# Kernel optimization log

Measured on AMD Instinct MI355X. Metric: run time of the kernel, lower is better.

## Reference

```python
import jax, jax.numpy as jnp
import numpy as np

DIM = 128; DSTATE = 64; DHEAD = 64; EXPAND = 2
DINNER = EXPAND * DIM; NH = DINNER // DHEAD
CONVK = 4; CHUNK = 128
BATCH = 1; DD = 32; HH = 32; WW = 32
CONVCH = DINNER + 2 * DSTATE
DPROJ = 2 * DINNER + 2 * DSTATE + NH


def rmsnorm(v, w, eps=1e-6):
    return v * jax.lax.rsqrt(jnp.mean(v * v, axis=-1, keepdims=True) + eps) * w


def ssd(xh, dt, A, Bm, Cm):
    # chunked SSD selective scan. xh [b,l,h,p], dt [b,l,h], A [h], Bm/Cm [b,l,n]
    b, l, h, p = xh.shape
    n = Bm.shape[-1]
    c, k = l // CHUNK, CHUNK
    dA = (dt * A).reshape(b, c, k, h)
    xdt = (xh * dt[..., None]).reshape(b, c, k, h, p)
    Bm = Bm.reshape(b, c, k, n)
    Cm = Cm.reshape(b, c, k, n)
    cum = jnp.cumsum(dA, axis=2)                  # [b,c,k,h] inclusive
    cum_h = cum.transpose(0, 1, 3, 2)             # [b,c,h,k]
    tri = jnp.tril(jnp.ones((k, k), bool))
    Lmat = jnp.exp(jnp.where(tri, cum_h[..., :, None] - cum_h[..., None, :], -jnp.inf))
    CB = jnp.einsum('bctn,bcsn->bcts', Cm, Bm)
    Y_intra = jnp.einsum('bcts,bchts,bcshp->bcthp', CB, Lmat, xdt)
    decay_end = jnp.exp(cum[:, :, -1:, :] - cum)  # [b,c,k,h]
    S = jnp.einsum('bcsn,bcsh,bcshp->bchpn', Bm, decay_end, xdt)
    cdec = jnp.exp(cum[:, :, -1])                 # [b,c,h]

    def step(hprev, inp):
        s_c, dec = inp
        return dec[:, :, None, None] * hprev + s_c, hprev

    init = jnp.zeros((b, h, p, n), xh.dtype)
    _, hprevs = jax.lax.scan(step, init, (S.transpose(1, 0, 2, 3, 4), cdec.transpose(1, 0, 2)))
    hprevs = hprevs.transpose(1, 0, 2, 3, 4)      # [b,c,h,p,n] state at each chunk start
    Y_inter = jnp.einsum('bctn,bcth,bchpn->bcthp', Cm, jnp.exp(cum), hprevs)
    return (Y_intra + Y_inter).reshape(b, l, h, p)


def mamba2(x, Win, convw, convb, dtb, Alog, Dp, normw, Wout):
    b, l, _ = x.shape
    zxbcdt = x @ Win
    z = zxbcdt[..., :DINNER]
    xBC = zxbcdt[..., DINNER:DINNER + CONVCH]
    dt = zxbcdt[..., DINNER + CONVCH:]
    xc = xBC.transpose(0, 2, 1)
    xc = jax.lax.conv_general_dilated(xc, convw, (1,), [(CONVK - 1, 0)],
                                      dimension_numbers=('NCH', 'OIH', 'NCH'),
                                      feature_group_count=CONVCH)
    xBC = jax.nn.silu(xc + convb[None, :, None]).transpose(0, 2, 1)
    xh = xBC[..., :DINNER].reshape(b, l, NH, DHEAD)
    Bm = xBC[..., DINNER:DINNER + DSTATE]
    Cm = xBC[..., DINNER + DSTATE:]
    dt = jax.nn.softplus(dt + dtb)
    A = -jnp.exp(Alog)
    y = ssd(xh, dt, A, Bm, Cm) + Dp[None, None, :, None] * xh
    y = y.reshape(b, l, DINNER)
    y = rmsnorm(y * jax.nn.silu(z), normw)
    return y @ Wout


def ss3d(xn, gate_w, gate_b, ps, pn, pz):
    B, D, H, W, C = xn.shape
    x_s = xn.reshape(B, -1, C)
    x_n = jnp.transpose(xn, (0, 2, 1, 3, 4)).reshape(B, -1, C)
    x_z = jnp.transpose(xn, (0, 3, 1, 2, 4)).reshape(B, -1, C)
    o_sf = mamba2(x_s, *ps).reshape(B, D, H, W, C)
    o_sb = jnp.flip(mamba2(jnp.flip(x_s, 1), *ps), 1).reshape(B, D, H, W, C)
    o_nf = mamba2(x_n, *pn).reshape(B, H, D, W, C).transpose(0, 2, 1, 3, 4)
    o_nb = jnp.flip(mamba2(jnp.flip(x_n, 1), *pn), 1).reshape(B, H, D, W, C).transpose(0, 2, 1, 3, 4)
    o_zf = mamba2(x_z, *pz).reshape(B, W, D, H, C).transpose(0, 2, 3, 1, 4)
    o_zb = jnp.flip(mamba2(jnp.flip(x_z, 1), *pz), 1).reshape(B, W, D, H, C).transpose(0, 2, 3, 1, 4)
    stack = jnp.stack([o_sf, o_sb, o_nf, o_nb, o_zf, o_zb], axis=1)  # [B,6,D,H,W,C]
    gates = jax.nn.softmax(xn @ gate_w + gate_b, axis=-1)            # [B,D,H,W,6]
    gates = jnp.transpose(gates[..., None], (0, 4, 1, 2, 3, 5))      # [B,6,D,H,W,1]
    return (stack * gates).sum(axis=1)


def block(x, norm_w, gate_w, gate_b, ps, pn, pz, loc_dw_w, loc_dw_b, loc_pw_w, loc_pw_b,
          ca_w1, ca_b1, ca_w2, ca_b2, alpha):
    xp = jnp.transpose(x, (0, 2, 3, 4, 1))
    xn = rmsnorm(xp, norm_w)
    g = jnp.transpose(ss3d(xn, gate_w, gate_b, ps, pn, pz), (0, 4, 1, 2, 3))
    xcf = jnp.transpose(xn, (0, 4, 1, 2, 3))
    lc = jax.lax.conv_general_dilated(xcf, loc_dw_w, (1, 1, 1), [(1, 1)] * 3,
                                      dimension_numbers=('NCDHW', 'OIDHW', 'NCDHW'),
                                      feature_group_count=DIM) + loc_dw_b[None, :, None, None, None]
    lc = jax.nn.silu(jnp.einsum('bcdhw,oc->bodhw', lc, loc_pw_w) + loc_pw_b[None, :, None, None, None])
    fused = alpha * g + (1.0 - alpha) * lc
    yc = jnp.mean(fused, axis=(2, 3, 4), keepdims=True)
    yc = jnp.einsum('bcdhw,oc->bodhw', yc, ca_w1) + ca_b1[None, :, None, None, None]
    yc = jnp.where(yc >= 0, yc, 0.1 * yc)  # LeakyReLU(0.1)
    yc = jnp.einsum('bcdhw,oc->bodhw', yc, ca_w2) + ca_b2[None, :, None, None, None]
    return x + fused * jax.nn.sigmoid(yc)


def setup_inputs() -> dict:
    keys = iter(jax.random.split(jax.random.key(0), 64))

    def rn(shape, s=1.0):
        return jax.random.normal(next(keys), shape, jnp.float32) * s

    inp = {"x": rn((BATCH, DIM, DD, HH, WW))}
    inp["norm_w"] = jnp.ones((DIM,)) + rn((DIM,), 0.02)
    inp["gate_w"] = rn((DIM, 6), 0.02)
    inp["gate_b"] = jnp.zeros((6,))
    for m in ("s", "n", "zm"):
        inp[m + "_Win"] = rn((DIM, DPROJ), 0.02)
        inp[m + "_convw"] = rn((CONVCH, 1, CONVK), 0.2)
        inp[m + "_convb"] = jnp.zeros((CONVCH,))
        inp[m + "_dtb"] = rn((NH,), 0.3)
        inp[m + "_Alog"] = jnp.log(jnp.arange(1, NH + 1, dtype=jnp.float32))
        inp[m + "_D"] = jnp.ones((NH,))
        inp[m + "_normw"] = jnp.ones((DINNER,))
        inp[m + "_Wout"] = rn((DINNER, DIM), 0.02)
    inp["loc_dw_w"] = rn((DIM, 1, 3, 3, 3), 0.1)
    inp["loc_dw_b"] = jnp.zeros((DIM,))
    inp["loc_pw_w"] = rn((DIM, DIM), 0.05)
    inp["loc_pw_b"] = jnp.zeros((DIM,))
    inp["ca_w1"] = rn((DIM // 16, DIM), 0.05)
    inp["ca_b1"] = jnp.zeros((DIM // 16,))
    inp["ca_w2"] = rn((DIM, DIM // 16), 0.05)
    inp["ca_b2"] = jnp.zeros((DIM,))
    inp["alpha"] = jnp.array(0.5, jnp.float32)
    return inp


def reference(x, norm_w, gate_w, gate_b,
              s_Win, s_convw, s_convb, s_dtb, s_Alog, s_D, s_normw, s_Wout,
              n_Win, n_convw, n_convb, n_dtb, n_Alog, n_D, n_normw, n_Wout,
              zm_Win, zm_convw, zm_convb, zm_dtb, zm_Alog, zm_D, zm_normw, zm_Wout,
              loc_dw_w, loc_dw_b, loc_pw_w, loc_pw_b, ca_w1, ca_b1, ca_w2, ca_b2, alpha):
    ps = (s_Win, s_convw, s_convb, s_dtb, s_Alog, s_D, s_normw, s_Wout)
    pn = (n_Win, n_convw, n_convb, n_dtb, n_Alog, n_D, n_normw, n_Wout)
    pz = (zm_Win, zm_convw, zm_convb, zm_dtb, zm_Alog, zm_D, zm_normw, zm_Wout)
    return block(x, norm_w, gate_w, gate_b, ps, pn, pz,
                 loc_dw_w, loc_dw_b, loc_pw_w, loc_pw_b, ca_w1, ca_b1, ca_w2, ca_b2, alpha)
```

## Files before the change

### kernel.cpp

```cpp
#include <hip/hip_runtime.h>


typedef unsigned short u16;
typedef unsigned int   u32;
typedef __attribute__((ext_vector_type(8))) short short8;
typedef __attribute__((ext_vector_type(8))) _Float16 half8;
typedef __attribute__((ext_vector_type(4))) float f32x4;

#define LSEQ 32768
#define CDIM 128
#define NPROJ 644
#define CCH 384
#define DIN 256
#define NHD 4
#define CKL 128
#define NCHK 256

__device__ __forceinline__ float b2f(u16 u){ u32 x=((u32)u)<<16; float f; __builtin_memcpy(&f,&x,4); return f; }
__device__ __forceinline__ u16 f2b(float f){ u32 x; __builtin_memcpy(&x,&f,4); x += 0x7fffu + ((x>>16)&1u); return (u16)(x>>16); }
__device__ __forceinline__ u16 f2h(float v){ _Float16 h=(_Float16)v; u16 b; __builtin_memcpy(&b,&h,2); return b; }
__device__ __forceinline__ float h2f(u16 b){ _Float16 h; __builtin_memcpy(&h,&b,2); return (float)h; }
__device__ __forceinline__ void up4(uint2 v, float* o){
  union { uint2 u; _Float16 h[4]; } c; c.u = v;
  o[0]=(float)c.h[0]; o[1]=(float)c.h[1]; o[2]=(float)c.h[2]; o[3]=(float)c.h[3];
}
__device__ __forceinline__ uint2 pk4(const float* o){
  union { uint2 u; _Float16 h[4]; } c;
  c.h[0]=(_Float16)o[0]; c.h[1]=(_Float16)o[1]; c.h[2]=(_Float16)o[2]; c.h[3]=(_Float16)o[3];
  return c.u;
}
__device__ __forceinline__ float sigmoidf_(float v){ return 1.f/(1.f+__expf(-v)); }
__device__ __forceinline__ float siluf_(float v){ return v*sigmoidf_(v); }
__device__ __forceinline__ float softplusf_(float v){ return (v>20.f)? v : log1pf(__expf(v)); }

__device__ __forceinline__ int seq2sp(int t, int run){
  int te = (run&1) ? (LSEQ-1-t) : t;
  int a = te>>10, b=(te>>5)&31, c=te&31;
  int d,h,w;
  switch(run>>1){
    case 0: d=a; h=b; w=c; break;
    case 1: h=a; d=b; w=c; break;
    default: w=a; d=b; h=c; break;
  }
  return (d<<10)|(h<<5)|w;
}

__global__ void k_xn(const float* __restrict__ x, const float* __restrict__ nw,
                     const float* __restrict__ gw, const float* __restrict__ gb,
                     float* __restrict__ XN, float* __restrict__ G){
  int s = blockIdx.x*256 + threadIdx.x;
  float ss = 0.f;
  #pragma unroll 8
  for (int c=0;c<CDIM;c++){ float v=x[c*LSEQ+s]; ss += v*v; }
  float sc = rsqrtf(ss*(1.f/CDIM)+1e-6f);
  float a[6];
  #pragma unroll
  for (int j=0;j<6;j++) a[j]=gb[j];
  #pragma unroll 8
  for (int c=0;c<CDIM;c++){
    float v = x[c*LSEQ+s]*sc*nw[c];
    XN[c*LSEQ+s] = v;
    #pragma unroll
    for (int j=0;j<6;j++) a[j] += v*gw[c*6+j];
  }
  float m=a[0];
  #pragma unroll
  for (int j=1;j<6;j++) m = fmaxf(m,a[j]);
  float e[6], ssum=0.f;
  #pragma unroll
  for (int j=0;j<6;j++){ e[j]=__expf(a[j]-m); ssum+=e[j]; }
  float inv = 1.f/ssum;
  #pragma unroll
  for (int j=0;j<6;j++) G[j*LSEQ+s] = e[j]*inv;
}

__global__ __launch_bounds__(256) void k_permute(const float* __restrict__ XN, u16* __restrict__ XNT, int dir){
  __shared__ u16 TS[128*34];
  int a = blockIdx.x>>5, b = blockIdx.x&31;
  int tid = threadIdx.x;
  int spa = (dir==1)? b : a;
  int spb = (dir==1)? a : b;
  int spbase = spa*1024 + spb*32;
  for (int idx=tid; idx<4096; idx+=256){
    int c = idx>>5, i = idx&31;
    TS[c*34+i] = f2b(XN[c*LSEQ + spbase + i]);
  }
  __syncthreads();
  for (int idx=tid; idx<4096; idx+=256){
    int i = idx>>7, c = idx&127;
    int t = (dir==2) ? (i*1024 + a*32 + b) : (a*1024 + b*32 + i);
    XNT[t*128 + c] = TS[c*34+i];
  }
}

__global__ void k_prep(const float* __restrict__ Win, const float* __restrict__ Wout,
                       u16* __restrict__ WinT, u16* __restrict__ WoT){
  int bid = blockIdx.x;
  if (bid < 384){
    int idx = bid*256 + threadIdx.x;
    int j = idx>>7, k = idx&127;
    float v = (j<NPROJ)? Win[k*NPROJ + j] : 0.f;
    WinT[idx] = f2b(v);
  } else {
    int idx = (bid-384)*256 + threadIdx.x;
    int c = idx>>8, k = idx&255;
    WoT[idx] = f2h(Wout[k*CDIM + c]);
  }
}

__global__ __launch_bounds__(256) void k_gin_mfma(const u16* __restrict__ XNT, const u16* __restrict__ WinT,
                                                  u16* __restrict__ ZX, int flip){
  __shared__ u16 Asb[128*136];
  __shared__ u16 Bsb[128*136];
  int j0 = blockIdx.x*128, t0 = blockIdx.y*128;
  int tid = threadIdx.x;
  for (int ch = tid; ch < 2048; ch += 256){
    int row = ch>>4, c8 = ch&15;
    int tg = flip ? (LSEQ-1-(t0+row)) : (t0+row);
    uint4 av = *(const uint4*)(XNT + tg*128 + c8*8);
    *(uint4*)(&Asb[row*136 + c8*8]) = av;
    uint4 bv = *(const uint4*)(WinT + (j0+row)*128 + c8*8);
    *(uint4*)(&Bsb[row*136 + c8*8]) = bv;
  }
  __syncthreads();
  int lane = tid&63, wid = tid>>6;
  int wm = (wid>>1)*64, wn = (wid&1)*64;
  int lm = lane&15, lq = lane>>4;
  f32x4 acc[4][4] = {};
  for (int kt=0; kt<4; kt++){
    short8 af[4], bf[4];
    #pragma unroll
    for (int mt=0;mt<4;mt++) af[mt] = *(const short8*)(&Asb[(wm+mt*16+lm)*136 + kt*32 + lq*8]);
    #pragma unroll
    for (int nt=0;nt<4;nt++) bf[nt] = *(const short8*)(&Bsb[(wn+nt*16+lm)*136 + kt*32 + lq*8]);
    #pragma unroll
    for (int mt=0;mt<4;mt++)
      #pragma unroll
      for (int nt=0;nt<4;nt++)
        acc[mt][nt] = __builtin_amdgcn_mfma_f32_16x16x32_bf16(af[mt], bf[nt], acc[mt][nt], 0,0,0);
  }
  #pragma unroll
  for (int mt=0;mt<4;mt++){
    #pragma unroll
    for (int nt=0;nt<4;nt++){
      int j = j0 + wn + nt*16 + lm;
      if (j < NPROJ){
        #pragma unroll
        for (int r=0;r<4;r++){
          int t = t0 + wm + mt*16 + lq*4 + r;
          ZX[t*NPROJ + j] = f2h(acc[mt][nt][r]);
        }
      }
    }
  }
}

__global__ __launch_bounds__(384) void k_conv(const u16* __restrict__ ZX, const float* __restrict__ cw,
                                              const float* __restrict__ cb, u16* __restrict__ XB){
  __shared__ u16 smc[35*384];
  int t0 = blockIdx.x*32;
  int tid = threadIdx.x;
  for (int idx=tid; idx<13440; idx+=384){
    int j = idx/384, chh = idx - j*384;
    int t = t0-3+j;
    smc[idx] = (t>=0)? ZX[t*NPROJ + 256 + chh] : (u16)0;
  }
  __syncthreads();
  int ch = tid;
  float w0=cw[ch*4], w1=cw[ch*4+1], w2=cw[ch*4+2], w3=cw[ch*4+3], bb=cb[ch];
  for (int i=0;i<32;i++){
    float acc = w0*h2f(smc[i*384+ch]) + w1*h2f(smc[(i+1)*384+ch])
              + w2*h2f(smc[(i+2)*384+ch]) + w3*h2f(smc[(i+3)*384+ch]) + bb;
    XB[(t0+i)*CCH + ch] = f2h(siluf_(acc));
  }
}

__global__ __launch_bounds__(256) void k_dtcum(const u16* __restrict__ ZX, const float* __restrict__ dtb,
                                               const float* __restrict__ Alog, float* __restrict__ DT,
                                               float* __restrict__ CUM, float* __restrict__ CDEC,
                                               float* __restrict__ DE){
  int g = blockIdx.x*4 + (threadIdx.x>>6);
  int lane = threadIdx.x&63;
  int c = g>>2, h = g&3;
  float A = -__expf(Alog[h]);
  float bias = dtb[h];
  int t0 = c*CKL + lane*2;
  float x0 = h2f(ZX[t0*NPROJ + 640 + h]);
  float x1 = h2f(ZX[(t0+1)*NPROJ + 640 + h]);
  float d0 = softplusf_(x0+bias), d1 = softplusf_(x1+bias);
  DT[t0*4+h] = d0; DT[(t0+1)*4+h] = d1;
  float e0 = d0*A, e1 = d1*A;
  float s = e0+e1;
  #pragma unroll
  for (int off=1; off<64; off<<=1){
    float v = __shfl_up(s, off, 64);
    if (lane>=off) s += v;
  }
  float c0 = s - e1, c1 = s;
  CUM[t0*4+h] = c0;
  CUM[(t0+1)*4+h] = c1;
  float tot = __shfl(s, 63, 64);
  DE[t0*4+h]     = __expf(tot - c0);
  DE[(t0+1)*4+h] = __expf(tot - c1);
  if (lane==0) CDEC[c*4+h] = __expf(tot);
}

__global__ __launch_bounds__(256,4) void k_chunk(const u16* __restrict__ XB, const float* __restrict__ DT,
                                                 const float* __restrict__ CUM, const float* __restrict__ DE,
                                                 const float* __restrict__ Dp,
                                                 u16* __restrict__ YA, u16* __restrict__ ST){
  __shared__ u16 sh[19968];
  u16* R0   = sh;
  u16* Mtri = sh;
  u16* Xsh  = sh + 11264;

  int bid = blockIdx.x; int c = bid&255, h = bid>>8;
  int tid = threadIdx.x, lane = tid&63, wid = tid>>6;
  int lm = lane&15, lq = lane>>4;
  const u16* XBc = XB + c*CKL*CCH;
  const float* DTc = DT + c*CKL*4 + h;
  const float* DEc = DE + c*CKL*4 + h;

  for (int idx=tid; idx<4096; idx+=256){
    int t2 = idx>>6, n = idx&63, t = t2*2;
    const u16* r0 = XBc + t*CCH;
    float dt0 = DTc[t*4], dt1 = DTc[(t+1)*4];
    u32 xp = (u32)f2h(h2f(r0[(h<<6)+n])*dt0) | ((u32)f2h(h2f(r0[CCH+(h<<6)+n])*dt1)<<16);
    *(u32*)&Xsh[n*136 + t] = xp;
    float de0 = DEc[t*4], de1 = DEc[(t+1)*4];
    u32 bp = (u32)f2h(h2f(r0[256+n])*de0) | ((u32)f2h(h2f(r0[CCH+256+n])*de1)<<16);
    *(u32*)&R0[n*136 + t] = bp;
  }
  if (tid<128) ((float*)(Xsh + (tid>>1)*136 + 128))[tid&1] = CUM[(c*CKL+tid)*4 + h];
  __syncthreads();
  #define CUMS(t) (((const float*)(Xsh + ((t)>>1)*136 + 128))[(t)&1])

  f32x4 sa[4] = {};
  #pragma unroll
  for (int kt=0; kt<4; kt++){
    half8 aa = *(const half8*)&Xsh[(wid*16+lm)*136 + kt*32 + lq*8];
    #pragma unroll
    for (int nt=0;nt<4;nt++){
      half8 bq = *(const half8*)&R0[(nt*16+lm)*136 + kt*32 + lq*8];
      sa[nt] = __builtin_amdgcn_mfma_f32_16x16x32_f16(aa, bq, sa[nt], 0,0,0);
    }
  }
  #pragma unroll
  for (int nt=0;nt<4;nt++){
    int n = nt*16 + lm;
    #pragma unroll
    for (int r=0;r<4;r++){
      int p = wid*16 + lq*4 + r;
      ST[((c*4+h)*64 + p)*64 + n] = f2h(sa[nt][r]);
    }
  }

  int sp0 = wid, sp1 = 7 - wid;
  f32x4 cbA[4] = {};
  f32x4 cbB[8] = {};
  const u16* lanebase = XBc + lm*CCH + lq*8;
  #pragma unroll
  for (int kt=0; kt<2; kt++){
    half8 afA = *(const half8*)(lanebase + sp0*16*CCH + 320 + kt*32);
    half8 afB = *(const half8*)(lanebase + sp1*16*CCH + 320 + kt*32);
    #pragma unroll
    for (int st=0; st<8; st++){
      if (st <= sp1){
        half8 bq = *(const half8*)(lanebase + st*16*CCH + 256 + kt*32);
        if (st <= sp0)
          cbA[st&3] = __builtin_amdgcn_mfma_f32_16x16x32_f16(afA, bq, cbA[st&3], 0,0,0);
        cbB[st] = __builtin_amdgcn_mfma_f32_16x16x32_f16(afB, bq, cbB[st], 0,0,0);
      }
    }
  }
  __syncthreads();

  float dval = Dp[h];
  #pragma unroll
  for (int i=0;i<2;i++){
    int sp_ = i ? sp1 : sp0;
    int q = sp_ >> 1;
    int Wst = 32*q + 40;
    int mb  = 16*(32*q*q + 48*q + (sp_&1)*(32*q+40));
    u16* Mrow = Mtri + mb;
    float ct[4];
    #pragma unroll
    for (int r=0;r<4;r++) ct[r] = CUMS(sp_*16 + lq*4 + r);

    #pragma unroll
    for (int st=0; st<8; st++){
      if (st <= sp_){
        int s = st*16 + lm;
        float cs = CUMS(s);
        f32x4 cb;
        if (i==0) cb = cbA[st&3]; else cb = cbB[st];
        if (st == sp_){
          #pragma unroll
          for (int r=0;r<4;r++){
            int t = sp_*16 + lq*4 + r;
            float m = (s <= t) ? cb[r]*__expf(ct[r]-cs) : 0.f;
            Mrow[(lq*4+r)*Wst + s] = f2h(m);
          }
          if (!(sp_&1)){
            #pragma unroll
            for (int r=0;r<4;r++) Mrow[(lq*4+r)*Wst + s + 16] = 0;
          }
        } else {
          #pragma unroll
          for (int r=0;r<4;r++)
            Mrow[(lq*4+r)*Wst + s] = f2h(cb[r]*__expf(ct[r]-cs));
        }
      }
    }

    f32x4 ya[4] = {};
    int nkt = q + 1;
    #pragma unroll
    for (int kt=0; kt<4; kt++){
      if (kt < nkt){
        half8 af = *(const half8*)&Mrow[lm*Wst + kt*32 + lq*8];
        #pragma unroll
        for (int nt=0;nt<4;nt++){
          half8 bq = *(const half8*)&Xsh[(nt*16+lm)*136 + kt*32 + lq*8];
          ya[nt] = __builtin_amdgcn_mfma_f32_16x16x32_f16(af, bq, ya[nt], 0,0,0);
        }
      }
    }

    #pragma unroll
    for (int nt=0;nt<4;nt++){
      int p = nt*16 + lm;
      #pragma unroll
      for (int r=0;r<4;r++){
        int t = sp_*16 + lq*4 + r;
        float xhv = h2f(XBc[t*CCH + (h<<6) + p]);
        YA[((c*CKL+t)<<8) + (h<<6) + p] = f2h(ya[nt][r] + dval*xhv);
      }
    }
  }
  #undef CUMS
}

__global__ void k_scan(const u16* __restrict__ ST, u16* __restrict__ HP, const float* __restrict__ CDEC){
  int g = blockIdx.x*256 + threadIdx.x;
  int h = g>>12;
  float hp = 0.f;
  #pragma unroll 32
  for (int c=0;c<NCHK;c++){
    float dec = CDEC[(c<<2)+h];
    float sv = h2f(ST[g + (c<<14)]);
    HP[g + (c<<14)] = f2h(hp);
    hp = dec*hp + sv;
  }
}

__global__ __launch_bounds__(256) void k_inter(const u16* __restrict__ XB, const float* __restrict__ CUM,
                                               const u16* __restrict__ HP, u16* __restrict__ YB){
  __shared__ u16 Cs[128*72];
  __shared__ u16 Hs[4*64*72];
  __shared__ float ex_s[4*128];
  int c = blockIdx.x;
  int tid = threadIdx.x, lane = tid&63, wid = tid>>6;
  int lm = lane&15, lq = lane>>4;
  for (int idx=tid; idx<1024; idx+=256){
    int t = idx>>3, b8 = idx&7;
    *(uint4*)&Cs[t*72 + b8*8] = *(const uint4*)(XB + (c*CKL+t)*CCH + 320 + b8*8);
  }
  for (int idx=tid; idx<2048; idx+=256){
    int h = idx>>9, p = (idx>>3)&63, b8 = idx&7;
    *(uint4*)&Hs[(h*64+p)*72 + b8*8] = *(const uint4*)(HP + ((c*4+h)*64+p)*64 + b8*8);
  }
  for (int idx=tid; idx<512; idx+=256){
    int h = idx>>7, t = idx&127;
    ex_s[h*128+t] = __expf(CUM[(c*CKL+t)*4+h]);
  }
  __syncthreads();
  int h = wid;
  const u16* Hh = &Hs[h*64*72];
  f32x4 acc[8][4] = {};
  for (int kt=0; kt<2; kt++){
    half8 af[8], bfv[4];
    #pragma unroll
    for (int mt=0;mt<8;mt++) af[mt] = *(const half8*)&Cs[(mt*16+lm)*72 + kt*32 + lq*8];
    #pragma unroll
    for (int nt=0;nt<4;nt++) bfv[nt] = *(const half8*)&Hh[(nt*16+lm)*72 + kt*32 + lq*8];
    #pragma unroll
    for (int mt=0;mt<8;mt++)
      #pragma unroll
      for (int nt=0;nt<4;nt++)
        acc[mt][nt] = __builtin_amdgcn_mfma_f32_16x16x32_f16(af[mt], bfv[nt], acc[mt][nt], 0,0,0);
  }
  #pragma unroll
  for (int mt=0;mt<8;mt++){
    #pragma unroll
    for (int r=0;r<4;r++){
      int t = mt*16 + lq*4 + r;
      float e = ex_s[h*128+t];
      u16* dst = &YB[((c*CKL+t)<<8) + (h<<6)];
      #pragma unroll
      for (int nt=0;nt<4;nt++){
        int p = nt*16 + lm;
        dst[p] = f2h(e*acc[mt][nt][r]);
      }
    }
  }
}

__global__ __launch_bounds__(256) void k_gout_mfma(const u16* __restrict__ YA, const u16* __restrict__ YB,
                                                   const u16* __restrict__ ZX, const float* __restrict__ nw,
                                                   const u16* __restrict__ WoT,
                                                   const float* __restrict__ G, float* __restrict__ GACC, int run){
  __shared__ u16 Ys[128*136];
  __shared__ u16 Ws[128*136];
  __shared__ float SSs[128];
  int t0 = blockIdx.x*128;
  int tid = threadIdx.x, lane = tid&63, wid = tid>>6;
  int lm = lane&15, lq = lane>>4;
  f32x4 acc[2][8] = {};
  for (int kb=0; kb<2; kb++){
    __syncthreads();
    for (int ch=tid; ch<2048; ch+=256){
      int row = ch>>4, c8 = ch&15;
      int t = t0+row;
      int cb = kb*128 + c8*8;
      uint2 av0 = *(const uint2*)(YA + t*DIN + cb);
      uint2 av1 = *(const uint2*)(YA + t*DIN + cb + 4);
      uint2 bv0 = *(const uint2*)(YB + t*DIN + cb);
      uint2 bv1 = *(const uint2*)(YB + t*DIN + cb + 4);
      uint2 zv0 = *(const uint2*)(ZX + t*NPROJ + cb);
      uint2 zv1 = *(const uint2*)(ZX + t*NPROJ + cb + 4);
      float af[8], bf[8], zf[8];
      up4(av0, af); up4(av1, af+4);
      up4(bv0, bf); up4(bv1, bf+4);
      up4(zv0, zf); up4(zv1, zf+4);
      float ssp = 0.f;
      union { uint4 u; u16 h[8]; } pk;
      #pragma unroll
      for (int j=0;j<8;j++){
        float u = (af[j]+bf[j])*siluf_(zf[j]);
        ssp += u*u;
        pk.h[j] = f2h(u*nw[cb+j]);
      }
      *(uint4*)&Ys[row*136 + c8*8] = pk.u;
      *(uint4*)&Ws[row*136 + c8*8] = *(const uint4*)(WoT + row*DIN + kb*128 + c8*8);
      #pragma unroll
      for (int off=1; off<16; off<<=1) ssp += __shfl_xor(ssp, off, 64);
      if ((lane&15)==0){ if (kb==0) SSs[row] = ssp; else SSs[row] += ssp; }
    }
    __syncthreads();
    for (int kt=0; kt<4; kt++){
      half8 af[2], bfv[8];
      #pragma unroll
      for (int mt=0;mt<2;mt++) af[mt] = *(const half8*)&Ys[(wid*32+mt*16+lm)*136 + kt*32 + lq*8];
      #pragma unroll
      for (int nt=0;nt<8;nt++) bfv[nt] = *(const half8*)&Ws[(nt*16+lm)*136 + kt*32 + lq*8];
      #pragma unroll
      for (int mt=0;mt<2;mt++)
        #pragma unroll
        for (int nt=0;nt<8;nt++)
          acc[mt][nt] = __builtin_amdgcn_mfma_f32_16x16x32_f16(af[mt], bfv[nt], acc[mt][nt], 0,0,0);
    }
  }
  #pragma unroll
  for (int mt=0;mt<2;mt++){
    #pragma unroll
    for (int r=0;r<4;r++){
      int tl = wid*32 + mt*16 + lq*4 + r;
      int t = t0 + tl;
      int sp = seq2sp(t, run);
      float sc = rsqrtf(SSs[tl]*(1.f/DIN)+1e-6f);
      float g = G[run*LSEQ + sp] * sc;
      float* dst = &GACC[sp*CDIM];
      if (run==0){
        #pragma unroll
        for (int nt=0;nt<8;nt++) dst[nt*16+lm] = g*acc[mt][nt][r];
      } else {
        #pragma unroll
        for (int nt=0;nt<8;nt++) dst[nt*16+lm] += g*acc[mt][nt][r];
      }
    }
  }
}

__global__ __launch_bounds__(256) void k_dwconv(const float* __restrict__ XN, const float* __restrict__ w,
                                                const float* __restrict__ b, float* __restrict__ LC1){
  __shared__ float sm[3*34*40];
  int cc = blockIdx.x>>5, d = blockIdx.x&31;
  int tid = threadIdx.x;
  for (int i=tid; i<4080; i+=256) sm[i] = 0.f;
  __syncthreads();
  #pragma unroll
  for (int p=0;p<3;p++){
    int dz = d-1+p;
    if ((unsigned)dz<=31u){
      for (int idx=tid; idx<1024; idx+=256){
        int hh = idx>>5, ww = idx&31;
        sm[p*1360 + (hh+1)*40 + (ww+4)] = XN[cc*LSEQ + (dz<<10) + idx];
      }
    }
  }
  __syncthreads();
  float wreg[27];
  #pragma unroll
  for (int i=0;i<27;i++) wreg[i] = w[cc*27+i];
  float bias = b[cc];
  int h = tid>>3, w0 = (tid&7)*4;
  float4 acc = {bias,bias,bias,bias};
  #pragma unroll
  for (int p=0;p<3;p++){
    #pragma unroll
    for (int dy=0;dy<3;dy++){
      const float* row = &sm[p*1360 + (h+dy)*40 + 4];
      float left  = row[w0-1];
      float4 mid  = *(const float4*)&row[w0];
      float right = row[w0+4];
      float wa=wreg[p*9+dy*3+0], wb=wreg[p*9+dy*3+1], wc=wreg[p*9+dy*3+2];
      acc.x += wa*left  + wb*mid.x + wc*mid.y;
      acc.y += wa*mid.x + wb*mid.y + wc*mid.z;
      acc.z += wa*mid.y + wb*mid.z + wc*mid.w;
      acc.w += wa*mid.z + wb*mid.w + wc*right;
    }
  }
  *(float4*)&LC1[cc*LSEQ + (d<<10) + h*32 + w0] = acc;
}

__global__ __launch_bounds__(256) void k_pw(const float* __restrict__ LC1, const float* __restrict__ pw,
                                            const float* __restrict__ pwb, float* __restrict__ LC2){
  __shared__ u16 Ws[128*136];
  __shared__ u16 Bs[128*136];
  int s0 = blockIdx.x*128;
  int tid = threadIdx.x, lane = tid&63, wid = tid>>6;
  int lm = lane&15, lq = lane>>4;
  for (int idx=tid; idx<16384; idx+=256){
    int o = idx>>7, cc = idx&127;
    Ws[o*136+cc] = f2h(pw[idx]);
  }
  for (int idx=tid; idx<16384; idx+=256){
    int cc = idx>>7, n = idx&127;
    Bs[n*136+cc] = f2h(LC1[cc*LSEQ + s0 + n]);
  }
  __syncthreads();
  f32x4 acc[2][8] = {};
  for (int kt=0; kt<4; kt++){
    half8 af[2], bfv[8];
    #pragma unroll
    for (int mt=0;mt<2;mt++) af[mt] = *(const half8*)&Ws[(wid*32+mt*16+lm)*136 + kt*32 + lq*8];
    #pragma unroll
    for (int nt=0;nt<8;nt++) bfv[nt] = *(const half8*)&Bs[(nt*16+lm)*136 + kt*32 + lq*8];
    #pragma unroll
    for (int mt=0;mt<2;mt++)
      #pragma unroll
      for (int nt=0;nt<8;nt++)
        acc[mt][nt] = __builtin_amdgcn_mfma_f32_16x16x32_f16(af[mt], bfv[nt], acc[mt][nt], 0,0,0);
  }
  #pragma unroll
  for (int mt=0;mt<2;mt++){
    #pragma unroll
    for (int r=0;r<4;r++){
      int o = wid*32 + mt*16 + lq*4 + r;
      float bb = pwb[o];
      float* dst = &LC2[o*LSEQ + s0];
      #pragma unroll
      for (int nt=0;nt<8;nt++){
        int n = nt*16 + lm;
        dst[n] = siluf_(acc[mt][nt][r] + bb);
      }
    }
  }
}

__global__ void k_fuse(const float* __restrict__ GACC, const float* __restrict__ LC2,
                       const float* __restrict__ alpha, float* __restrict__ FUSED){
  __shared__ float tile[64*65];
  int bs = blockIdx.x>>1, bc = blockIdx.x&1;
  int s0 = bs*64, c0 = bc*64;
  int tid = threadIdx.x;
  float a = alpha[0];
  for (int idx=tid; idx<4096; idx+=256){
    int i = idx>>6, j = idx&63;
    tile[i*65+j] = GACC[(s0+i)*CDIM + c0+j];
  }
  __syncthreads();
  for (int idx=tid; idx<4096; idx+=256){
    int j = idx>>6, i = idx&63;
    float g = tile[i*65+j];
    float l = LC2[(c0+j)*LSEQ + s0+i];
    FUSED[(c0+j)*LSEQ + s0+i] = a*g + (1.f-a)*l;
  }
}

__global__ void k_mean(const float* __restrict__ F, float* __restrict__ MEAN){
  __shared__ float red[4];
  int cc = blockIdx.x, tid = threadIdx.x;
  float acc = 0.f;
  for (int s=tid; s<LSEQ; s+=256) acc += F[cc*LSEQ + s];
  #pragma unroll
  for (int off=32; off; off>>=1) acc += __shfl_down(acc, off, 64);
  if ((tid&63)==0) red[tid>>6] = acc;
  __syncthreads();
  if (tid==0) MEAN[cc] = (red[0]+red[1]+red[2]+red[3])*(1.f/LSEQ);
}

__global__ void k_ca(const float* __restrict__ MEAN, const float* __restrict__ w1, const float* __restrict__ b1,
                     const float* __restrict__ w2, const float* __restrict__ b2, float* __restrict__ SIG){
  __shared__ float y1[8];
  int tid = threadIdx.x;
  if (tid<8){
    float acc = b1[tid];
    for (int c=0;c<128;c++) acc += w1[tid*128+c]*MEAN[c];
    y1[tid] = (acc>=0.f)? acc : 0.1f*acc;
  }
  __syncthreads();
  float acc = b2[tid];
  #pragma unroll
  for (int o=0;o<8;o++) acc += w2[tid*8+o]*y1[o];
  SIG[tid] = sigmoidf_(acc);
}

__global__ void k_final(const float* __restrict__ x, const float* __restrict__ F, const float* __restrict__ SIG,
                        float* __restrict__ out){
  int idx = blockIdx.x*256 + threadIdx.x;
  int cc = idx>>15;
  out[idx] = x[idx] + F[idx]*SIG[cc];
}

extern "C" void kernel_launch(void* const* d_in, const int* in_sizes, int n_in,
                              void* d_out, int out_size, void* d_ws, size_t ws_size,
                              hipStream_t stream){
  (void)in_sizes; (void)n_in; (void)out_size; (void)ws_size;
  const float* x       = (const float*)d_in[0];
  const float* norm_w  = (const float*)d_in[1];
  const float* gate_w  = (const float*)d_in[2];
  const float* gate_b  = (const float*)d_in[3];
  const float* loc_dw_w= (const float*)d_in[28];
  const float* loc_dw_b= (const float*)d_in[29];
  const float* loc_pw_w= (const float*)d_in[30];
  const float* loc_pw_b= (const float*)d_in[31];
  const float* ca_w1   = (const float*)d_in[32];
  const float* ca_b1   = (const float*)d_in[33];
  const float* ca_w2   = (const float*)d_in[34];
  const float* ca_b2   = (const float*)d_in[35];
  const float* alpha   = (const float*)d_in[36];

  float* W     = (float*)d_ws;
  float* XN    = W;
  float* GATES = XN    + 4194304;
  float* GACC  = GATES + 196608;
  u16*   ZX    = (u16*)(GACC + 4194304);
  u16*   XB    = (u16*)(GACC + 4194304 + 10551296);
  float* DT    = GACC + 4194304 + 10551296 + 6291456;
  float* CUM   = DT    + 131072;
  float* CDEC  = CUM   + 131072;
  float* DE    = CDEC  + 1024;
  float* STreg = DE    + 131072;
  float* Y     = STreg + 4194304;
  float* LC1   = Y     + 8388608;
  float* LC2   = LC1   + 4194304;
  float* MEAN  = LC2   + 4194304;
  float* SIG   = MEAN  + 128;
  u16*   XNT   = (u16*)(SIG + 128);
  u16*   WinT  = XNT + 4194304;
  u16*   WoT   = WinT + 98304;
  u16*   ST16  = (u16*)STreg;
  u16*   YA    = (u16*)Y;
  u16*   YB    = YA + 8388608;
  u16*   HP16  = (u16*)LC1;

  k_xn<<<128,256,0,stream>>>(x, norm_w, gate_w, gate_b, XN, GATES);

  for (int r=0;r<6;r++){
    int m = r>>1;
    const float* Win   = (const float*)d_in[4 + m*8 + 0];
    const float* convw = (const float*)d_in[4 + m*8 + 1];
    const float* convb = (const float*)d_in[4 + m*8 + 2];
    const float* dtb   = (const float*)d_in[4 + m*8 + 3];
    const float* Alog  = (const float*)d_in[4 + m*8 + 4];
    const float* Dp    = (const float*)d_in[4 + m*8 + 5];
    const float* nw2   = (const float*)d_in[4 + m*8 + 6];
    const float* Wout  = (const float*)d_in[4 + m*8 + 7];
    if ((r&1)==0){
      k_permute<<<1024,256,0,stream>>>(XN, XNT, m);
      k_prep   <<<512,256,0,stream>>>(Win, Wout, WinT, WoT);
    }
    k_gin_mfma<<<dim3(6,256),256,0,stream>>>(XNT, WinT, ZX, r&1);
    k_conv    <<<1024,384,0,stream>>>(ZX, convw, convb, XB);
    k_dtcum   <<<256,256,0,stream>>>(ZX, dtb, Alog, DT, CUM, CDEC, DE);
    k_chunk   <<<1024,256,0,stream>>>(XB, DT, CUM, DE, Dp, YA, ST16);
    k_scan    <<<64,256,0,stream>>>(ST16, HP16, CDEC);
    k_inter   <<<256,256,0,stream>>>(XB, CUM, HP16, YB);
    k_gout_mfma<<<256,256,0,stream>>>(YA, YB, ZX, nw2, WoT, GATES, GACC, r);
  }

  k_dwconv<<<4096,256,0,stream>>>(XN, loc_dw_w, loc_dw_b, LC1);
  k_pw    <<<256,256,0,stream>>>(LC1, loc_pw_w, loc_pw_b, LC2);
  k_fuse  <<<1024,256,0,stream>>>(GACC, LC2, alpha, LC1);
  k_mean  <<<128,256,0,stream>>>(LC1, MEAN);
  k_ca    <<<1,128,0,stream>>>(MEAN, ca_w1, ca_b1, ca_w2, ca_b2, SIG);
  k_final <<<16384,256,0,stream>>>(x, LC1, SIG, (float*)d_out);
}
```

Baseline: 1.017 ms.

## Merge small kernels, pad ZX row stride, swizzle GEMM tiles, fuse mean into fuse

Merges permute and weight prep into one launch, and conv with the dt cumulative-sum kernel into another. It pads the ZX row stride from 644 to 672 for aligned rows and remaps k_gin_mfma block indices to a swizzled 1D grid. It also computes per-channel partial sums inside k_fuse via wave reductions, so the separate k_mean pass is dropped and k_ca finishes the reduction. Together these cut launch count and global re-reads, at the cost of more workspace and a serial 512-element sum per thread in k_ca.

```diff
diff --git a/kernel.cpp b/kernel.cpp
--- a/kernel.cpp
+++ b/kernel.cpp
@@ -10,6 +10,7 @@
 #define LSEQ 32768
 #define CDIM 128
 #define NPROJ 644
+#define ZXS 672
 #define CCH 384
 #define DIN 256
 #define NHD 4
@@ -74,35 +75,34 @@
   for (int j=0;j<6;j++) G[j*LSEQ+s] = e[j]*inv;
 }
 
-__global__ __launch_bounds__(256) void k_permute(const float* __restrict__ XN, u16* __restrict__ XNT, int dir){
+__global__ __launch_bounds__(256) void k_permprep(const float* __restrict__ XN, u16* __restrict__ XNT, int dir,
+                                                  const float* __restrict__ Win, const float* __restrict__ Wout,
+                                                  u16* __restrict__ WinT, u16* __restrict__ WoT){
   __shared__ u16 TS[128*34];
-  int a = blockIdx.x>>5, b = blockIdx.x&31;
+  int bid = blockIdx.x;
   int tid = threadIdx.x;
-  int spa = (dir==1)? b : a;
-  int spb = (dir==1)? a : b;
-  int spbase = spa*1024 + spb*32;
-  for (int idx=tid; idx<4096; idx+=256){
-    int c = idx>>5, i = idx&31;
-    TS[c*34+i] = f2b(XN[c*LSEQ + spbase + i]);
-  }
-  __syncthreads();
-  for (int idx=tid; idx<4096; idx+=256){
-    int i = idx>>7, c = idx&127;
-    int t = (dir==2) ? (i*1024 + a*32 + b) : (a*1024 + b*32 + i);
-    XNT[t*128 + c] = TS[c*34+i];
-  }
-}
-
-__global__ void k_prep(const float* __restrict__ Win, const float* __restrict__ Wout,
-                       u16* __restrict__ WinT, u16* __restrict__ WoT){
-  int bid = blockIdx.x;
-  if (bid < 384){
-    int idx = bid*256 + threadIdx.x;
+  if (bid < 1024){
+    int a = bid>>5, b = bid&31;
+    int spa = (dir==1)? b : a;
+    int spb = (dir==1)? a : b;
+    int spbase = spa*1024 + spb*32;
+    for (int idx=tid; idx<4096; idx+=256){
+      int c = idx>>5, i = idx&31;
+      TS[c*34+i] = f2b(XN[c*LSEQ + spbase + i]);
+    }
+    __syncthreads();
+    for (int idx=tid; idx<4096; idx+=256){
+      int i = idx>>7, c = idx&127;
+      int t = (dir==2) ? (i*1024 + a*32 + b) : (a*1024 + b*32 + i);
+      XNT[t*128 + c] = TS[c*34+i];
+    }
+  } else if (bid < 1408){
+    int idx = (bid-1024)*256 + tid;
     int j = idx>>7, k = idx&127;
     float v = (j<NPROJ)? Win[k*NPROJ + j] : 0.f;
     WinT[idx] = f2b(v);
   } else {
-    int idx = (bid-384)*256 + threadIdx.x;
+    int idx = (bid-1408)*256 + tid;
     int c = idx>>8, k = idx&255;
     WoT[idx] = f2h(Wout[k*CDIM + c]);
   }
@@ -112,7 +112,10 @@
                                                   u16* __restrict__ ZX, int flip){
   __shared__ u16 Asb[128*136];
   __shared__ u16 Bsb[128*136];
-  int j0 = blockIdx.x*128, t0 = blockIdx.y*128;
+  int g = blockIdx.x;
+  int w = (g&7)*192 + (g>>3);
+  int by = w/6, bx = w - by*6;
+  int j0 = bx*128, t0 = by*128;
   int tid = threadIdx.x;
   for (int ch = tid; ch < 2048; ch += 256){
     int row = ch>>4, c8 = ch&15;
@@ -148,61 +151,62 @@
         #pragma unroll
         for (int r=0;r<4;r++){
           int t = t0 + wm + mt*16 + lq*4 + r;
-          ZX[t*NPROJ + j] = f2h(acc[mt][nt][r]);
+          ZX[t*ZXS + j] = f2h(acc[mt][nt][r]);
         }
       }
     }
   }
 }
 
-__global__ __launch_bounds__(384) void k_conv(const u16* __restrict__ ZX, const float* __restrict__ cw,
-                                              const float* __restrict__ cb, u16* __restrict__ XB){
+__global__ __launch_bounds__(384) void k_convdt(const u16* __restrict__ ZX, const float* __restrict__ cw,
+                                                const float* __restrict__ cb, u16* __restrict__ XB,
+                                                const float* __restrict__ dtb, const float* __restrict__ Alog,
+                                                float* __restrict__ DT, float* __restrict__ CUM,
+                                                float* __restrict__ CDEC, float* __restrict__ DE){
   __shared__ u16 smc[35*384];
-  int t0 = blockIdx.x*32;
+  int bid = blockIdx.x;
   int tid = threadIdx.x;
-  for (int idx=tid; idx<13440; idx+=384){
-    int j = idx/384, chh = idx - j*384;
-    int t = t0-3+j;
-    smc[idx] = (t>=0)? ZX[t*NPROJ + 256 + chh] : (u16)0;
-  }
-  __syncthreads();
-  int ch = tid;
-  float w0=cw[ch*4], w1=cw[ch*4+1], w2=cw[ch*4+2], w3=cw[ch*4+3], bb=cb[ch];
-  for (int i=0;i<32;i++){
-    float acc = w0*h2f(smc[i*384+ch]) + w1*h2f(smc[(i+1)*384+ch])
-              + w2*h2f(smc[(i+2)*384+ch]) + w3*h2f(smc[(i+3)*384+ch]) + bb;
-    XB[(t0+i)*CCH + ch] = f2h(siluf_(acc));
-  }
-}
-
-__global__ __launch_bounds__(256) void k_dtcum(const u16* __restrict__ ZX, const float* __restrict__ dtb,
-                                               const float* __restrict__ Alog, float* __restrict__ DT,
-                                               float* __restrict__ CUM, float* __restrict__ CDEC,
-                                               float* __restrict__ DE){
-  int g = blockIdx.x*4 + (threadIdx.x>>6);
-  int lane = threadIdx.x&63;
-  int c = g>>2, h = g&3;
-  float A = -__expf(Alog[h]);
-  float bias = dtb[h];
-  int t0 = c*CKL + lane*2;
-  float x0 = h2f(ZX[t0*NPROJ + 640 + h]);
-  float x1 = h2f(ZX[(t0+1)*NPROJ + 640 + h]);
-  float d0 = softplusf_(x0+bias), d1 = softplusf_(x1+bias);
-  DT[t0*4+h] = d0; DT[(t0+1)*4+h] = d1;
-  float e0 = d0*A, e1 = d1*A;
-  float s = e0+e1;
-  #pragma unroll
-  for (int off=1; off<64; off<<=1){
-    float v = __shfl_up(s, off, 64);
-    if (lane>=off) s += v;
-  }
-  float c0 = s - e1, c1 = s;
-  CUM[t0*4+h] = c0;
-  CUM[(t0+1)*4+h] = c1;
-  float tot = __shfl(s, 63, 64);
-  DE[t0*4+h]     = __expf(tot - c0);
-  DE[(t0+1)*4+h] = __expf(tot - c1);
-  if (lane==0) CDEC[c*4+h] = __expf(tot);
+  if (bid < 1024){
+    int t0 = bid*32;
+    for (int idx=tid; idx<13440; idx+=384){
+      int j = idx/384, chh = idx - j*384;
+      int t = t0-3+j;
+      smc[idx] = (t>=0)? ZX[t*ZXS + 256 + chh] : (u16)0;
+    }
+    __syncthreads();
+    int ch = tid;
+    float w0=cw[ch*4], w1=cw[ch*4+1], w2=cw[ch*4+2], w3=cw[ch*4+3], bb=cb[ch];
+    for (int i=0;i<32;i++){
+      float acc = w0*h2f(smc[i*384+ch]) + w1*h2f(smc[(i+1)*384+ch])
+                + w2*h2f(smc[(i+2)*384+ch]) + w3*h2f(smc[(i+3)*384+ch]) + bb;
+      XB[(t0+i)*CCH + ch] = f2h(siluf_(acc));
+    }
+  } else if (tid < 256){
+    int g = (bid-1024)*4 + (tid>>6);
+    int lane = tid&63;
+    int c = g>>2, h = g&3;
+    float A = -__expf(Alog[h]);
+    float bias = dtb[h];
+    int t0 = c*CKL + lane*2;
+    float x0 = h2f(ZX[t0*ZXS + 640 + h]);
+    float x1 = h2f(ZX[(t0+1)*ZXS + 640 + h]);
+    float d0 = softplusf_(x0+bias), d1 = softplusf_(x1+bias);
+    DT[t0*4+h] = d0; DT[(t0+1)*4+h] = d1;
+    float e0 = d0*A, e1 = d1*A;
+    float s = e0+e1;
+    #pragma unroll
+    for (int off=1; off<64; off<<=1){
+      float v = __shfl_up(s, off, 64);
+      if (lane>=off) s += v;
+    }
+    float c0 = s - e1, c1 = s;
+    CUM[t0*4+h] = c0;
+    CUM[(t0+1)*4+h] = c1;
+    float tot = __shfl(s, 63, 64);
+    DE[t0*4+h]     = __expf(tot - c0);
+    DE[(t0+1)*4+h] = __expf(tot - c1);
+    if (lane==0) CDEC[c*4+h] = __expf(tot);
+  }
 }
 
 __global__ __launch_bounds__(256,4) void k_chunk(const u16* __restrict__ XB, const float* __restrict__ DT,
@@ -427,8 +431,8 @@
       uint2 av1 = *(const uint2*)(YA + t*DIN + cb + 4);
       uint2 bv0 = *(const uint2*)(YB + t*DIN + cb);
       uint2 bv1 = *(const uint2*)(YB + t*DIN + cb + 4);
-      uint2 zv0 = *(const uint2*)(ZX + t*NPROJ + cb);
-      uint2 zv1 = *(const uint2*)(ZX + t*NPROJ + cb + 4);
+      uint2 zv0 = *(const uint2*)(ZX + t*ZXS + cb);
+      uint2 zv1 = *(const uint2*)(ZX + t*ZXS + cb + 4);
       float af[8], bf[8], zf[8];
       up4(av0, af); up4(av1, af+4);
       up4(bv0, bf); up4(bv1, bf+4);
@@ -570,7 +574,8 @@
 }
 
 __global__ void k_fuse(const float* __restrict__ GACC, const float* __restrict__ LC2,
-                       const float* __restrict__ alpha, float* __restrict__ FUSED){
+                       const float* __restrict__ alpha, float* __restrict__ FUSED,
+                       float* __restrict__ MEANP){
   __shared__ float tile[64*65];
   int bs = blockIdx.x>>1, bc = blockIdx.x&1;
   int s0 = bs*64, c0 = bc*64;
@@ -585,29 +590,31 @@
     int j = idx>>6, i = idx&63;
     float g = tile[i*65+j];
     float l = LC2[(c0+j)*LSEQ + s0+i];
-    FUSED[(c0+j)*LSEQ + s0+i] = a*g + (1.f-a)*l;
-  }
-}
-
-__global__ void k_mean(const float* __restrict__ F, float* __restrict__ MEAN){
-  __shared__ float red[4];
-  int cc = blockIdx.x, tid = threadIdx.x;
-  float acc = 0.f;
-  for (int s=tid; s<LSEQ; s+=256) acc += F[cc*LSEQ + s];
-  #pragma unroll
-  for (int off=32; off; off>>=1) acc += __shfl_down(acc, off, 64);
-  if ((tid&63)==0) red[tid>>6] = acc;
-  __syncthreads();
-  if (tid==0) MEAN[cc] = (red[0]+red[1]+red[2]+red[3])*(1.f/LSEQ);
-}
-
-__global__ void k_ca(const float* __restrict__ MEAN, const float* __restrict__ w1, const float* __restrict__ b1,
+    float f = a*g + (1.f-a)*l;
+    FUSED[(c0+j)*LSEQ + s0+i] = f;
+    float wsum = f;
+    #pragma unroll
+    for (int off=32; off; off>>=1) wsum += __shfl_xor(wsum, off, 64);
+    if ((tid&63)==0) MEANP[(c0+j)*512 + bs] = wsum;
+  }
+}
+
+__global__ void k_ca(const float* __restrict__ MEANP, const float* __restrict__ w1, const float* __restrict__ b1,
                      const float* __restrict__ w2, const float* __restrict__ b2, float* __restrict__ SIG){
+  __shared__ float MEANsh[128];
   __shared__ float y1[8];
   int tid = threadIdx.x;
+  {
+    float acc = 0.f;
+    const float* p = MEANP + tid*512;
+    #pragma unroll 16
+    for (int b=0;b<512;b++) acc += p[b];
+    MEANsh[tid] = acc*(1.f/LSEQ);
+  }
+  __syncthreads();
   if (tid<8){
     float acc = b1[tid];
-    for (int c=0;c<128;c++) acc += w1[tid*128+c]*MEAN[c];
+    for (int c=0;c<128;c++) acc += w1[tid*128+c]*MEANsh[c];
     y1[tid] = (acc>=0.f)? acc : 0.1f*acc;
   }
   __syncthreads();
@@ -647,8 +654,8 @@
   float* GATES = XN    + 4194304;
   float* GACC  = GATES + 196608;
   u16*   ZX    = (u16*)(GACC + 4194304);
-  u16*   XB    = (u16*)(GACC + 4194304 + 10551296);
-  float* DT    = GACC + 4194304 + 10551296 + 6291456;
+  u16*   XB    = (u16*)(GACC + 4194304 + 11010048);
+  float* DT    = GACC + 4194304 + 11010048 + 6291456;
   float* CUM   = DT    + 131072;
   float* CDEC  = CUM   + 131072;
   float* DE    = CDEC  + 1024;
@@ -656,8 +663,8 @@
   float* Y     = STreg + 4194304;
   float* LC1   = Y     + 8388608;
   float* LC2   = LC1   + 4194304;
-  float* MEAN  = LC2   + 4194304;
-  float* SIG   = MEAN  + 128;
+  float* MEANP = LC2   + 4194304;
+  float* SIG   = MEANP + 65536;
   u16*   XNT   = (u16*)(SIG + 128);
   u16*   WinT  = XNT + 4194304;
   u16*   WoT   = WinT + 98304;
@@ -679,12 +686,10 @@
     const float* nw2   = (const float*)d_in[4 + m*8 + 6];
     const float* Wout  = (const float*)d_in[4 + m*8 + 7];
     if ((r&1)==0){
-      k_permute<<<1024,256,0,stream>>>(XN, XNT, m);
-      k_prep   <<<512,256,0,stream>>>(Win, Wout, WinT, WoT);
-    }
-    k_gin_mfma<<<dim3(6,256),256,0,stream>>>(XNT, WinT, ZX, r&1);
-    k_conv    <<<1024,384,0,stream>>>(ZX, convw, convb, XB);
-    k_dtcum   <<<256,256,0,stream>>>(ZX, dtb, Alog, DT, CUM, CDEC, DE);
+      k_permprep<<<1536,256,0,stream>>>(XN, XNT, m, Win, Wout, WinT, WoT);
+    }
+    k_gin_mfma<<<1536,256,0,stream>>>(XNT, WinT, ZX, r&1);
+    k_convdt  <<<1280,384,0,stream>>>(ZX, convw, convb, XB, dtb, Alog, DT, CUM, CDEC, DE);
     k_chunk   <<<1024,256,0,stream>>>(XB, DT, CUM, DE, Dp, YA, ST16);
     k_scan    <<<64,256,0,stream>>>(ST16, HP16, CDEC);
     k_inter   <<<256,256,0,stream>>>(XB, CUM, HP16, YB);
@@ -693,8 +698,7 @@
 
   k_dwconv<<<4096,256,0,stream>>>(XN, loc_dw_w, loc_dw_b, LC1);
   k_pw    <<<256,256,0,stream>>>(LC1, loc_pw_w, loc_pw_b, LC2);
-  k_fuse  <<<1024,256,0,stream>>>(GACC, LC2, alpha, LC1);
-  k_mean  <<<128,256,0,stream>>>(LC1, MEAN);
-  k_ca    <<<1,128,0,stream>>>(MEAN, ca_w1, ca_b1, ca_w2, ca_b2, SIG);
+  k_fuse  <<<1024,256,0,stream>>>(GACC, LC2, alpha, LC1, MEANP);
+  k_ca    <<<1,128,0,stream>>>(MEANP, ca_w1, ca_b1, ca_w2, ca_b2, SIG);
   k_final <<<16384,256,0,stream>>>(x, LC1, SIG, (float*)d_out);
 }
```

After: 941.6 us. 7.4% less time.
